# Performance work log

Measured on AMD Instinct MI355X. Metric: run time of the kernel, lower is better.

Reference implementation:

```python
import jax, jax.numpy as jnp
import numpy as np

SCALE_EPS = 1e-05


def _qweight(weight):
    # global abs-mean scale (detached), round-to-nearest-even, clamp to {-1,0,1}
    scale = SCALE_EPS + jax.lax.stop_gradient(jnp.mean(jnp.abs(weight)))
    quant = jnp.clip(jnp.round(weight / scale), -1.0, 1.0)
    # straight-through estimator: forward = quant, backward = identity on weight
    return weight + jax.lax.stop_gradient(quant - weight)


def setup_inputs() -> dict:
    key = jax.random.key(0)
    k_x, k_w = jax.random.split(key)
    B, S, IN, OUT = 4, 2048, 2048, 8192
    x = jax.random.normal(k_x, (B, S, IN), dtype=jnp.float32)
    weight = jax.random.normal(k_w, (OUT, IN), dtype=jnp.float32)
    bias = jnp.zeros((OUT,), dtype=jnp.float32)
    return {"x": x, "weight": weight, "bias": bias}


def reference(x, weight, bias):
    qw = _qweight(weight)  # ternary-valued (scaled forward value)
    # F.linear: x @ qw.T + bias ; [b,s,in] x [out,in] -> [b,s,out]
    return jnp.einsum('bsi,oi->bso', x, qw) + bias
```

## Files before the change

kernel.cpp:

```cpp
#include <hip/hip_runtime.h>
#include <hip/hip_bf16.h>

#define BM 128
#define BN 128
#define BK 32

typedef __attribute__((ext_vector_type(8))) short bf16x8;
typedef __attribute__((ext_vector_type(4))) float f32x4;

__device__ __forceinline__ unsigned short f2bf_rne(float f) {
  unsigned int u = __float_as_uint(f);
  u += 0x7FFFu + ((u >> 16) & 1u);
  return (unsigned short)(u >> 16);
}

__device__ __forceinline__ float bf2f(unsigned short h) {
  return __uint_as_float(((unsigned int)h) << 16);
}

__global__ void absmean_kernel(const float* __restrict__ w, long n, double* __restrict__ out) {
  double s = 0.0;
  long stride = (long)gridDim.x * blockDim.x * 4;
  for (long i = ((long)blockIdx.x * blockDim.x + threadIdx.x) * 4; i < n; i += stride) {
    float4 v = *(const float4*)(w + i);
    s += (double)fabsf(v.x) + (double)fabsf(v.y) + (double)fabsf(v.z) + (double)fabsf(v.w);
  }
  for (int o = 32; o > 0; o >>= 1) s += __shfl_down(s, o, 64);
  __shared__ double ls[4];
  int lane = threadIdx.x & 63, wv = threadIdx.x >> 6;
  if (lane == 0) ls[wv] = s;
  __syncthreads();
  if (threadIdx.x == 0) atomicAdd(out, ls[0] + ls[1] + ls[2] + ls[3]);
}

__global__ void prep_x_kernel(const float* __restrict__ x, unsigned short* __restrict__ xcat,
                              int K, int Kc, long n) {
  long stride = (long)gridDim.x * blockDim.x * 4;
  for (long i = ((long)blockIdx.x * blockDim.x + threadIdx.x) * 4; i < n; i += stride) {
    float4 v = *(const float4*)(x + i);
    float f[4] = {v.x, v.y, v.z, v.w};
    unsigned short hi[4], lo[4];
#pragma unroll
    for (int j = 0; j < 4; ++j) {
      hi[j] = f2bf_rne(f[j]);
      lo[j] = f2bf_rne(f[j] - bf2f(hi[j]));
    }
    long row = i / K;
    int col = (int)(i - row * K);
    unsigned short* p0 = xcat + row * (long)Kc + col;
    *(ushort4*)p0 = make_ushort4(hi[0], hi[1], hi[2], hi[3]);
    *(ushort4*)(p0 + K) = make_ushort4(lo[0], lo[1], lo[2], lo[3]);
  }
}

__global__ void prep_w_kernel(const float* __restrict__ w, unsigned short* __restrict__ wcat,
                              const double* __restrict__ sum, int K, int Kc, long n,
                              double inv_cnt) {
  float scale = 1e-5f + (float)(*sum * inv_cnt);
  long stride = (long)gridDim.x * blockDim.x * 4;
  for (long i = ((long)blockIdx.x * blockDim.x + threadIdx.x) * 4; i < n; i += stride) {
    float4 v = *(const float4*)(w + i);
    float f[4] = {v.x, v.y, v.z, v.w};
    unsigned short q[4];
#pragma unroll
    for (int j = 0; j < 4; ++j) {
      float t = f[j] / scale;
      t = rintf(t);
      t = fminf(1.0f, fmaxf(-1.0f, t));
      q[j] = f2bf_rne(t);
    }
    long row = i / K;
    int col = (int)(i - row * K);
    unsigned short* p0 = wcat + row * (long)Kc + col;
    *(ushort4*)p0 = make_ushort4(q[0], q[1], q[2], q[3]);
    *(ushort4*)(p0 + K) = make_ushort4(q[0], q[1], q[2], q[3]);
  }
}

__device__ __forceinline__ void gll16(const unsigned short* g, void* l) {
  __builtin_amdgcn_global_load_lds((const __attribute__((address_space(1))) unsigned int*)g,
                                   (__attribute__((address_space(3))) unsigned int*)l,
                                   16, 0, 0);
}

__global__ __launch_bounds__(256) void gemm_kernel(
    const unsigned short* __restrict__ A,
    const unsigned short* __restrict__ Bw,
    const float* __restrict__ bias,
    float* __restrict__ C, int M, int N, int Kc) {
  __shared__ __align__(16) unsigned short As[BM * BK];
  __shared__ __align__(16) unsigned short Bs[BN * BK];

  const int nbx = N / BN;
  const int nwg = (M / BM) * nbx;
  const int cpx = nwg >> 3;
  const int orig = blockIdx.x;
  const int wgid = (orig & 7) * cpx + (orig >> 3);
  const int bx = wgid % nbx;
  const int by = wgid / nbx;

  const int tid = threadIdx.x;
  const int lane = tid & 63;
  const int wv = tid >> 6;
  const int bm = by * BM;
  const int bn = bx * BN;
  const int wm = (wv >> 1) * 64;
  const int wn = (wv & 1) * 64;

  f32x4 acc[4][4] = {};

  const int srow = tid >> 2;
  const int scol = (tid & 3) * 8;
  const unsigned short* a0 = A + (size_t)(bm + srow) * Kc + scol;
  const unsigned short* a1 = A + (size_t)(bm + 64 + srow) * Kc + scol;
  const unsigned short* b0 = Bw + (size_t)(bn + srow) * Kc + scol;
  const unsigned short* b1 = Bw + (size_t)(bn + 64 + srow) * Kc + scol;
  char* asb = (char*)As + (size_t)wv * 1024;
  char* bsb = (char*)Bs + (size_t)wv * 1024;

  const int ar = (wm + (lane & 15)) * BK + (lane >> 4) * 8;
  const int br = (wn + (lane & 15)) * BK + (lane >> 4) * 8;

  for (int k0 = 0; k0 < Kc; k0 += BK) {
    gll16(a0 + k0, asb);
    gll16(a1 + k0, asb + 4096);
    gll16(b0 + k0, bsb);
    gll16(b1 + k0, bsb + 4096);
    __syncthreads();
    bf16x8 af[4], bfr[4];
#pragma unroll
    for (int t = 0; t < 4; ++t) {
      af[t] = *(const bf16x8*)(As + ar + t * 16 * BK);
      bfr[t] = *(const bf16x8*)(Bs + br + t * 16 * BK);
    }
#pragma unroll
    for (int i = 0; i < 4; ++i)
#pragma unroll
      for (int j = 0; j < 4; ++j)
        acc[i][j] = __builtin_amdgcn_mfma_f32_16x16x32_bf16(af[i], bfr[j], acc[i][j], 0, 0, 0);
    __syncthreads();
  }

  const int r0 = bm + wm + (lane >> 4) * 4;
  const int c0 = bn + wn + (lane & 15);
#pragma unroll
  for (int j = 0; j < 4; ++j) {
    const int col = c0 + j * 16;
    const float bv = bias[col];
#pragma unroll
    for (int i = 0; i < 4; ++i) {
#pragma unroll
      for (int r = 0; r < 4; ++r)
        C[(size_t)(r0 + i * 16 + r) * N + col] = acc[i][j][r] + bv;
    }
  }
}

__global__ void fallback_kernel(const float* __restrict__ x, const float* __restrict__ w,
                                const float* __restrict__ bias, const double* __restrict__ sum,
                                float* __restrict__ out, int M, int N, int K, double inv_cnt) {
  float scale = 1e-5f + (float)(*sum * inv_cnt);
  __shared__ float xs[64][33];
  __shared__ float qs[64][33];
  const int tid = threadIdx.x;
  const int bm = blockIdx.y * 64, bn = blockIdx.x * 64;
  const int ty = tid >> 4, tx = tid & 15;
  float acc[4][4] = {};
  for (int k0 = 0; k0 < K; k0 += 32) {
    for (int p = 0; p < 8; ++p) {
      int idx = p * 256 + tid;
      int r = idx >> 5, c = idx & 31;
      xs[r][c] = x[(size_t)(bm + r) * K + k0 + c];
      float t = w[(size_t)(bn + r) * K + k0 + c] / scale;
      t = rintf(t);
      qs[r][c] = fminf(1.0f, fmaxf(-1.0f, t));
    }
    __syncthreads();
    for (int kk = 0; kk < 32; ++kk) {
      float a[4], b[4];
#pragma unroll
      for (int i = 0; i < 4; ++i) a[i] = xs[ty * 4 + i][kk];
#pragma unroll
      for (int j = 0; j < 4; ++j) b[j] = qs[tx * 4 + j][kk];
#pragma unroll
      for (int i = 0; i < 4; ++i)
#pragma unroll
        for (int j = 0; j < 4; ++j) acc[i][j] += a[i] * b[j];
    }
    __syncthreads();
  }
#pragma unroll
  for (int i = 0; i < 4; ++i)
#pragma unroll
    for (int j = 0; j < 4; ++j)
      out[(size_t)(bm + ty * 4 + i) * N + bn + tx * 4 + j] = acc[i][j] + bias[bn + tx * 4 + j];
}

extern "C" void kernel_launch(void* const* d_in, const int* in_sizes, int n_in,
                              void* d_out, int out_size, void* d_ws, size_t ws_size,
                              hipStream_t stream) {
  const float* x = (const float*)d_in[0];
  const float* w = (const float*)d_in[1];
  const float* bias = (const float*)d_in[2];
  float* out = (float*)d_out;

  const int K = 2048;
  const int M = in_sizes[0] / K;
  const int N = in_sizes[2];
  const int Kc = 2 * K;
  const long nw = (long)N * K;
  const long nx = (long)M * K;
  const double inv_cnt = 1.0 / (double)nw;

  double* sum = (double*)d_ws;
  hipMemsetAsync(d_ws, 0, sizeof(double), stream);
  absmean_kernel<<<2048, 256, 0, stream>>>(w, nw, sum);

  size_t need = 256 + ((size_t)M + (size_t)N) * (size_t)Kc * sizeof(unsigned short);
  if (ws_size >= need) {
    unsigned short* xcat = (unsigned short*)((char*)d_ws + 256);
    unsigned short* wcat = xcat + (size_t)M * Kc;
    prep_x_kernel<<<2048, 256, 0, stream>>>(x, xcat, K, Kc, nx);
    prep_w_kernel<<<2048, 256, 0, stream>>>(w, wcat, sum, K, Kc, nw, inv_cnt);
    int nwg = (M / BM) * (N / BN);
    gemm_kernel<<<nwg, 256, 0, stream>>>(xcat, wcat, bias, out, M, N, Kc);
  } else {
    dim3 grid(N / 64, M / 64);
    fallback_kernel<<<grid, 256, 0, stream>>>(x, w, bias, sum, out, M, N, K, inv_cnt);
  }
}
```

Baseline: 1.095 ms.

## Rewrite GEMM as 256x256 tile, 8-wave kernel with 4-stage LDS pipeline

Replaces the 128x128, 4-wave GEMM with a 256x256 tile kernel using 8 waves, a 4-deep multi-buffered LDS pipeline fed by global_load_lds, and XOR swizzling to avoid LDS bank conflicts. Loads are interleaved with MFMA phases through explicit barriers, waitcnts and setprio, and the XCD-aware block remap is generalised. The goal is to hide global-load latency and raise data reuse per tile. In exchange the kernel uses the full 128KB of LDS and more accumulator registers, which limits occupancy. The prep kernels also switch from division to shifts.

Result: faster. 927.0 us (-15.3%).

```diff
diff --git a/kernel.cpp b/kernel.cpp
--- a/kernel.cpp
+++ b/kernel.cpp
@@ -1,9 +1,5 @@
 #include <hip/hip_runtime.h>
 #include <hip/hip_bf16.h>
-
-#define BM 128
-#define BN 128
-#define BK 32
 
 typedef __attribute__((ext_vector_type(8))) short bf16x8;
 typedef __attribute__((ext_vector_type(4))) float f32x4;
@@ -34,7 +30,8 @@
 }
 
 __global__ void prep_x_kernel(const float* __restrict__ x, unsigned short* __restrict__ xcat,
-                              int K, int Kc, long n) {
+                              int kshift, long n) {
+  const int K = 1 << kshift;
   long stride = (long)gridDim.x * blockDim.x * 4;
   for (long i = ((long)blockIdx.x * blockDim.x + threadIdx.x) * 4; i < n; i += stride) {
     float4 v = *(const float4*)(x + i);
@@ -45,17 +42,18 @@
       hi[j] = f2bf_rne(f[j]);
       lo[j] = f2bf_rne(f[j] - bf2f(hi[j]));
     }
-    long row = i / K;
-    int col = (int)(i - row * K);
-    unsigned short* p0 = xcat + row * (long)Kc + col;
+    long row = i >> kshift;
+    int col = (int)(i & (K - 1));
+    unsigned short* p0 = xcat + (row << (kshift + 1)) + col;
     *(ushort4*)p0 = make_ushort4(hi[0], hi[1], hi[2], hi[3]);
     *(ushort4*)(p0 + K) = make_ushort4(lo[0], lo[1], lo[2], lo[3]);
   }
 }
 
 __global__ void prep_w_kernel(const float* __restrict__ w, unsigned short* __restrict__ wcat,
-                              const double* __restrict__ sum, int K, int Kc, long n,
+                              const double* __restrict__ sum, int kshift, long n,
                               double inv_cnt) {
+  const int K = 1 << kshift;
   float scale = 1e-5f + (float)(*sum * inv_cnt);
   long stride = (long)gridDim.x * blockDim.x * 4;
   for (long i = ((long)blockIdx.x * blockDim.x + threadIdx.x) * 4; i < n; i += stride) {
@@ -69,9 +67,9 @@
       t = fminf(1.0f, fmaxf(-1.0f, t));
       q[j] = f2bf_rne(t);
     }
-    long row = i / K;
-    int col = (int)(i - row * K);
-    unsigned short* p0 = wcat + row * (long)Kc + col;
+    long row = i >> kshift;
+    int col = (int)(i & (K - 1));
+    unsigned short* p0 = wcat + (row << (kshift + 1)) + col;
     *(ushort4*)p0 = make_ushort4(q[0], q[1], q[2], q[3]);
     *(ushort4*)(p0 + K) = make_ushort4(q[0], q[1], q[2], q[3]);
   }
@@ -83,75 +81,124 @@
                                    16, 0, 0);
 }
 
-__global__ __launch_bounds__(256) void gemm_kernel(
+__global__ __launch_bounds__(512) void gemm8p_kernel(
     const unsigned short* __restrict__ A,
     const unsigned short* __restrict__ Bw,
     const float* __restrict__ bias,
-    float* __restrict__ C, int M, int N, int Kc) {
-  __shared__ __align__(16) unsigned short As[BM * BK];
-  __shared__ __align__(16) unsigned short Bs[BN * BK];
-
-  const int nbx = N / BN;
-  const int nwg = (M / BM) * nbx;
-  const int cpx = nwg >> 3;
-  const int orig = blockIdx.x;
-  const int wgid = (orig & 7) * cpx + (orig >> 3);
+    float* __restrict__ C, int M, int N) {
+  constexpr int Kc = 4096;
+  constexpr int NT = 128;
+  __shared__ __align__(16) unsigned short lds[65536];
+
+  const int nbx = N >> 8;
+  const int nwg = (M >> 8) * nbx;
+  const int q8 = nwg >> 3, r8 = nwg & 7;
+  const int xcd = blockIdx.x & 7;
+  const int loc = blockIdx.x >> 3;
+  const int wgid = (xcd < r8 ? xcd * (q8 + 1) : r8 * (q8 + 1) + (xcd - r8) * q8) + loc;
   const int bx = wgid % nbx;
   const int by = wgid / nbx;
+  const int bm = by << 8;
+  const int bn = bx << 8;
 
   const int tid = threadIdx.x;
   const int lane = tid & 63;
-  const int wv = tid >> 6;
-  const int bm = by * BM;
-  const int bn = bx * BN;
-  const int wm = (wv >> 1) * 64;
-  const int wn = (wv & 1) * 64;
-
-  f32x4 acc[4][4] = {};
-
-  const int srow = tid >> 2;
-  const int scol = (tid & 3) * 8;
-  const unsigned short* a0 = A + (size_t)(bm + srow) * Kc + scol;
-  const unsigned short* a1 = A + (size_t)(bm + 64 + srow) * Kc + scol;
-  const unsigned short* b0 = Bw + (size_t)(bn + srow) * Kc + scol;
-  const unsigned short* b1 = Bw + (size_t)(bn + 64 + srow) * Kc + scol;
-  char* asb = (char*)As + (size_t)wv * 1024;
-  char* bsb = (char*)Bs + (size_t)wv * 1024;
-
-  const int ar = (wm + (lane & 15)) * BK + (lane >> 4) * 8;
-  const int br = (wn + (lane & 15)) * BK + (lane >> 4) * 8;
-
-  for (int k0 = 0; k0 < Kc; k0 += BK) {
-    gll16(a0 + k0, asb);
-    gll16(a1 + k0, asb + 4096);
-    gll16(b0 + k0, bsb);
-    gll16(b1 + k0, bsb + 4096);
-    __syncthreads();
-    bf16x8 af[4], bfr[4];
-#pragma unroll
-    for (int t = 0; t < 4; ++t) {
-      af[t] = *(const bf16x8*)(As + ar + t * 16 * BK);
-      bfr[t] = *(const bf16x8*)(Bs + br + t * 16 * BK);
-    }
-#pragma unroll
-    for (int i = 0; i < 4; ++i)
-#pragma unroll
-      for (int j = 0; j < 4; ++j)
-        acc[i][j] = __builtin_amdgcn_mfma_f32_16x16x32_bf16(af[i], bfr[j], acc[i][j], 0, 0, 0);
-    __syncthreads();
-  }
-
-  const int r0 = bm + wm + (lane >> 4) * 4;
-  const int c0 = bn + wn + (lane & 15);
-#pragma unroll
-  for (int j = 0; j < 4; ++j) {
-    const int col = c0 + j * 16;
+  const int wid = tid >> 6;
+  const int wr = wid >> 2;
+  const int wc = wid & 3;
+
+  f32x4 acc[8][4] = {};
+
+  const int strow = tid >> 2;
+  const int sslot = ((tid & 3) ^ ((tid >> 2) & 3)) * 8;
+  const unsigned short* sA0 = A + (size_t)(bm + strow) * Kc + sslot;
+  const unsigned short* sA1 = A + (size_t)(bm + 128 + strow) * Kc + sslot;
+  const unsigned short* sB0 = Bw + (size_t)(bn + strow) * Kc + sslot;
+  const unsigned short* sB1 = Bw + (size_t)(bn + 128 + strow) * Kc + sslot;
+  char* dA = (char*)lds + (size_t)wid * 1024;
+  char* dB = (char*)lds + 65536 + (size_t)wid * 1024;
+
+  const int scol = (((lane >> 4) ^ (lane & 3)) << 3);
+  const int aoff = (wr * 128 + (lane & 15)) * 32 + scol;
+  const int boff = 32768 + (wc * 64 + (lane & 15)) * 32 + scol;
+
+#pragma unroll
+  for (int p = 0; p < 3; ++p) {
+    gll16(sA0 + p * 32, dA + p * 16384);
+    gll16(sA1 + p * 32, dA + p * 16384 + 8192);
+    gll16(sB0 + p * 32, dB + p * 16384);
+    gll16(sB1 + p * 32, dB + p * 16384 + 8192);
+  }
+  asm volatile("s_waitcnt vmcnt(8)" ::: "memory");
+  __builtin_amdgcn_s_barrier();
+
+  bf16x8 a_[4], b_[4];
+  for (int t = 0; t < NT; ++t) {
+    const unsigned short* base = lds + (t & 3) * 8192;
+    const int sb = (t + 3) & 3;
+    const int sk = (t + 3) * 32;
+    const bool doStage = (t + 3) < NT;
+
+#pragma unroll
+    for (int mi = 0; mi < 4; ++mi)
+      a_[mi] = *(const bf16x8*)&base[aoff + mi * 512];
+#pragma unroll
+    for (int ni = 0; ni < 4; ++ni)
+      b_[ni] = *(const bf16x8*)&base[boff + ni * 512];
+    if (doStage) {
+      gll16(sA0 + sk, dA + sb * 16384);
+      gll16(sA1 + sk, dA + sb * 16384 + 8192);
+    }
+    __builtin_amdgcn_s_barrier();
+    asm volatile("s_waitcnt lgkmcnt(0)" ::: "memory");
+    __builtin_amdgcn_sched_barrier(0);
+    __builtin_amdgcn_s_setprio(1);
+#pragma unroll
+    for (int mi = 0; mi < 4; ++mi)
+#pragma unroll
+      for (int ni = 0; ni < 4; ++ni)
+        acc[mi][ni] = __builtin_amdgcn_mfma_f32_16x16x32_bf16(a_[mi], b_[ni], acc[mi][ni], 0, 0, 0);
+    __builtin_amdgcn_s_setprio(0);
+    __builtin_amdgcn_s_barrier();
+
+#pragma unroll
+    for (int mi = 0; mi < 4; ++mi)
+      a_[mi] = *(const bf16x8*)&base[aoff + (mi + 4) * 512];
+    if (doStage) {
+      gll16(sB0 + sk, dB + sb * 16384);
+      gll16(sB1 + sk, dB + sb * 16384 + 8192);
+    }
+    __builtin_amdgcn_s_barrier();
+    asm volatile("s_waitcnt lgkmcnt(0)" ::: "memory");
+    __builtin_amdgcn_sched_barrier(0);
+    __builtin_amdgcn_s_setprio(1);
+#pragma unroll
+    for (int mi = 0; mi < 4; ++mi)
+#pragma unroll
+      for (int ni = 0; ni < 4; ++ni)
+        acc[mi + 4][ni] = __builtin_amdgcn_mfma_f32_16x16x32_bf16(a_[mi], b_[ni], acc[mi + 4][ni], 0, 0, 0);
+    __builtin_amdgcn_s_setprio(0);
+    if (t < NT - 3) {
+      asm volatile("s_waitcnt vmcnt(8)" ::: "memory");
+    } else if (t == NT - 3) {
+      asm volatile("s_waitcnt vmcnt(4)" ::: "memory");
+    } else if (t == NT - 2) {
+      asm volatile("s_waitcnt vmcnt(0)" ::: "memory");
+    }
+    __builtin_amdgcn_s_barrier();
+  }
+
+  const int r0 = bm + wr * 128 + (lane >> 4) * 4;
+  const int c0 = bn + wc * 64 + (lane & 15);
+#pragma unroll
+  for (int ni = 0; ni < 4; ++ni) {
+    const int col = c0 + ni * 16;
     const float bv = bias[col];
 #pragma unroll
-    for (int i = 0; i < 4; ++i) {
-#pragma unroll
-      for (int r = 0; r < 4; ++r)
-        C[(size_t)(r0 + i * 16 + r) * N + col] = acc[i][j][r] + bv;
+    for (int mi = 0; mi < 8; ++mi) {
+#pragma unroll
+      for (int rr = 0; rr < 4; ++rr)
+        C[(size_t)(r0 + mi * 16 + rr) * N + col] = acc[mi][ni][rr] + bv;
     }
   }
 }
@@ -205,6 +252,7 @@
   float* out = (float*)d_out;
 
   const int K = 2048;
+  const int kshift = 11;
   const int M = in_sizes[0] / K;
   const int N = in_sizes[2];
   const int Kc = 2 * K;
@@ -217,13 +265,14 @@
   absmean_kernel<<<2048, 256, 0, stream>>>(w, nw, sum);
 
   size_t need = 256 + ((size_t)M + (size_t)N) * (size_t)Kc * sizeof(unsigned short);
-  if (ws_size >= need) {
+  bool shapes_ok = (K == 2048) && ((M & 255) == 0) && ((N & 255) == 0);
+  if (shapes_ok && ws_size >= need) {
     unsigned short* xcat = (unsigned short*)((char*)d_ws + 256);
     unsigned short* wcat = xcat + (size_t)M * Kc;
-    prep_x_kernel<<<2048, 256, 0, stream>>>(x, xcat, K, Kc, nx);
-    prep_w_kernel<<<2048, 256, 0, stream>>>(w, wcat, sum, K, Kc, nw, inv_cnt);
-    int nwg = (M / BM) * (N / BN);
-    gemm_kernel<<<nwg, 256, 0, stream>>>(xcat, wcat, bias, out, M, N, Kc);
+    prep_x_kernel<<<2048, 256, 0, stream>>>(x, xcat, kshift, nx);
+    prep_w_kernel<<<2048, 256, 0, stream>>>(w, wcat, sum, kshift, nw, inv_cnt);
+    int nwg = (M >> 8) * (N >> 8);
+    gemm8p_kernel<<<nwg, 512, 0, stream>>>(xcat, wcat, bias, out, M, N);
   } else {
     dim3 grid(N / 64, M / 64);
     fallback_kernel<<<grid, 256, 0, stream>>>(x, w, bias, sum, out, M, N, K, inv_cnt);
```
